# Performance work log

Measured on AMD Instinct MI355X. Metric: run time of the kernel, lower is better.

Reference implementation:

```python
import jax, jax.numpy as jnp
import numpy as np

N_ITER = 5          # n_iterations
EPS_VAR = 1e-6      # added to var (both in update_likelihoods and after M-step)
EPS = 1e-7          # division guard in M-step


def setup_inputs() -> dict:
    key = jax.random.key(0)
    B, N, K, F = 8, 80000, 5, 20
    k1, k2 = jax.random.split(key)
    data = jax.random.normal(k1, (B, N, F), dtype=jnp.float32)
    # initialize_parameters: means are randomly sampled data points
    idx = jax.random.randint(k2, (B, K), 0, N)
    means = jnp.take_along_axis(data, idx[:, :, None], axis=1)          # [B,K,F]
    variance = jnp.ones((B, K, F), dtype=jnp.float32)                    # covariance_init=1.0
    prior = jnp.full((B, K), 1.0 / K, dtype=jnp.float32)
    return {"data": data, "means": means, "variance": variance, "prior": prior}


def _log_likelihoods(data, means, var, pi):
    # data [B,N,F], means/var [B,K,F], pi [B,K] -> [B,K,N]
    inv_cov = 1.0 / (var + EPS_VAR)                                       # [B,K,F]
    diff = data[:, None, :, :] - means[:, :, None, :]                     # [B,K,N,F]
    maha = jnp.einsum('bknf,bkf->bkn', diff * diff, inv_cov)              # bmm in torch
    coeff = -0.5 * jnp.log(2.0 * np.pi * var).sum(axis=-1)                # [B,K]
    return jnp.log(pi)[:, :, None] + coeff[:, :, None] - 0.5 * maha


def _posteriors(log_lik):
    # stable softmax over the cluster dim (dim=1), identical to update_posteriors
    return jax.nn.softmax(log_lik, axis=1)


def _m_step(post, data):
    # post [B,K,N], data [B,N,F]; weights == 1.0 branch of update_parameters
    n = data.shape[1]
    sizes = post.sum(axis=2, keepdims=True)                               # [B,K,1] cluster sizes
    pi = sizes[..., 0] / n                                                # [B,K]
    pi = pi / jnp.maximum(jnp.abs(pi).sum(axis=-1, keepdims=True), 1e-12) # L1 normalize
    means = jnp.einsum('bkn,bnf->bkf', post, data) / (sizes + EPS)        # [B,K,F]
    diff = data[:, None, :, :] - means[:, :, None, :]                     # [B,K,N,F]
    var = jnp.einsum('bkn,bknf->bkf', post, diff * diff) / (sizes + EPS)
    return means, var, pi


def reference(data, means, variance, prior):
    var, pi = variance, prior
    for _ in range(N_ITER):
        ll = _log_likelihoods(data, means, var, pi)
        post = _posteriors(ll)
        means, var, pi = _m_step(post, data)
        var = var + EPS_VAR
    ll = _log_likelihoods(data, means, var, pi)
    post = _posteriors(ll)
    # outputs permuted to [B, N, K] as in forward()
    return (jnp.transpose(ll, (0, 2, 1)), jnp.transpose(post, (0, 2, 1)), means, var, pi)
```

## Files before the change

### kernel.cpp

```cpp
#include <hip/hip_runtime.h>
#include <math.h>

#define BB 8
#define NPTS 80000
#define KK 5
#define FF 20
#define GG 128
#define TILE 64
#define NTILES (NPTS / TILE)
#define PSTRIDE 48

#define WS_CM 0
#define WS_CV 800
#define WS_CP 1600
#define WS_A  1640
#define WS_D  1680
#define WS_E  2480

#define WAIT_BAR() asm volatile("s_waitcnt lgkmcnt(0)\n\ts_barrier" ::: "memory")

__device__ __forceinline__ void make_coefs(const float* __restrict__ means,
                                           const float* __restrict__ var,
                                           const float* __restrict__ pi,
                                           float* __restrict__ A, float* __restrict__ D,
                                           float* __restrict__ E, int t) {
    if (t < BB * KK) {
        float sumlog = 0.f, summ2 = 0.f;
        for (int f = 0; f < FF; ++f) {
            float v = var[t * FF + f];
            float m = means[t * FF + f];
            float ic = 1.f / (v + 1e-6f);
            sumlog += logf(6.283185307179586f * v);
            summ2  += ic * m * m;
            D[t * FF + f] = ic * m;
            E[t * FF + f] = -0.5f * ic;
        }
        A[t] = logf(pi[t]) - 0.5f * sumlog - 0.5f * summ2;
    }
}

__global__ void prepare_kernel(const float* __restrict__ means, const float* __restrict__ var,
                               const float* __restrict__ pi, float* __restrict__ ws) {
    make_coefs(means, var, pi, ws + WS_A, ws + WS_D, ws + WS_E, (int)threadIdx.x);
}

template <bool WRITE_OUT>
__global__ __launch_bounds__(320) void estep_kernel(const float* __restrict__ data,
                                                    const float* __restrict__ ws,
                                                    float* __restrict__ partials,
                                                    float* __restrict__ out_ll,
                                                    float* __restrict__ out_post) {
    __shared__ float lls[2][KK][TILE];

    const int b    = blockIdx.x / GG;
    const int g    = blockIdx.x % GG;
    const int tid  = threadIdx.x;
    const int w    = __builtin_amdgcn_readfirstlane(tid >> 6);
    const int lane = tid & 63;

    const float* A = ws + WS_A;
    const float* D = ws + WS_D;
    const float* E = ws + WS_E;

    const float Ak = A[b * KK + w];
    float dk[FF], ek[FF];
#pragma unroll
    for (int f = 0; f < FF; ++f) {
        dk[f] = D[(b * KK + w) * FF + f];
        ek[f] = E[(b * KK + w) * FF + f];
    }

    float s0 = 0.f, s1[FF], s2[FF];
    if (!WRITE_OUT) {
#pragma unroll
        for (int f = 0; f < FF; ++f) { s1[f] = 0.f; s2[f] = 0.f; }
    }

    const float* dbase = data + (size_t)b * NPTS * FF;
    int pb = 0;

    for (int t = g; t < NTILES; t += GG) {
        const float* xp = dbase + ((size_t)t * TILE + lane) * FF;
        float4 xa = ((const float4*)xp)[0];
        float4 xb = ((const float4*)xp)[1];
        float4 xc = ((const float4*)xp)[2];
        float4 xd = ((const float4*)xp)[3];
        float4 xe = ((const float4*)xp)[4];

        float pf = 0.f;
        const int tn = t + GG;
        if (tn < NTILES) pf = dbase[((size_t)tn * TILE + lane) * FF];

        float x[FF];
        x[0]=xa.x; x[1]=xa.y; x[2]=xa.z; x[3]=xa.w;
        x[4]=xb.x; x[5]=xb.y; x[6]=xb.z; x[7]=xb.w;
        x[8]=xc.x; x[9]=xc.y; x[10]=xc.z; x[11]=xc.w;
        x[12]=xd.x; x[13]=xd.y; x[14]=xd.z; x[15]=xd.w;
        x[16]=xe.x; x[17]=xe.y; x[18]=xe.z; x[19]=xe.w;

        float za = 0.f, zb = 0.f;
#pragma unroll
        for (int f = 0; f < FF; f += 2) {
            za = fmaf(x[f],     fmaf(ek[f],     x[f],     dk[f]),     za);
            zb = fmaf(x[f + 1], fmaf(ek[f + 1], x[f + 1], dk[f + 1]), zb);
        }
        float z = Ak + za + zb;

        lls[pb][w][lane] = z;
        WAIT_BAR();

        float l0 = lls[pb][0][lane], l1 = lls[pb][1][lane], l2 = lls[pb][2][lane],
              l3 = lls[pb][3][lane], l4 = lls[pb][4][lane];
        float mx = fmaxf(fmaxf(fmaxf(l0, l1), fmaxf(l2, l3)), l4);
        float e0 = __expf(l0 - mx), e1 = __expf(l1 - mx), e2 = __expf(l2 - mx),
              e3 = __expf(l3 - mx), e4 = __expf(l4 - mx);
        float inv = 1.f / (e0 + e1 + e2 + e3 + e4);
        float ew  = (w == 0) ? e0 : (w == 1) ? e1 : (w == 2) ? e2 : (w == 3) ? e3 : e4;
        float post = ew * inv;

        if (WRITE_OUT) {
            size_t o = ((size_t)b * NPTS + (size_t)t * TILE + lane) * KK + w;
            out_ll[o]   = z;
            out_post[o] = post;
        } else {
            s0 += post;
#pragma unroll
            for (int f = 0; f < FF; ++f) {
                float px = post * x[f];
                s1[f] += px;
                s2[f] = fmaf(px, x[f], s2[f]);
            }
        }
        asm volatile("" :: "v"(pf));
        pb ^= 1;
    }

    if (!WRITE_OUT) {
#pragma unroll
        for (int off = 32; off > 0; off >>= 1) {
            s0 += __shfl_down(s0, off);
#pragma unroll
            for (int f = 0; f < FF; ++f) {
                s1[f] += __shfl_down(s1[f], off);
                s2[f] += __shfl_down(s2[f], off);
            }
        }
        if (lane == 0) {
            float* row = partials + ((size_t)(b * KK + w) * GG + g) * PSTRIDE;
#pragma unroll
            for (int f = 0; f < FF; ++f) { row[f] = s1[f]; row[FF + f] = s2[f]; }
            row[2 * FF] = s0;
        }
    }
}

__global__ __launch_bounds__(512) void update_kernel(const float* __restrict__ partials,
                                                     float* __restrict__ ws,
                                                     float* __restrict__ om,
                                                     float* __restrict__ ov,
                                                     float* __restrict__ op,
                                                     int write_params) {
    __shared__ float shA[8][PSTRIDE];
    __shared__ float shB[8 * KK];
    const int bk   = blockIdx.x;
    const int b    = bk / KK;
    const int tid  = threadIdx.x;
    const int w8   = tid >> 6;
    const int lane = tid & 63;

    if (lane < PSTRIDE) {
        const float* base = partials + (size_t)bk * GG * PSTRIDE + lane;
        float sv = 0.f;
        for (int gg = w8; gg < GG; gg += 8) sv += base[(size_t)gg * PSTRIDE];
        shA[w8][lane] = sv;
    }
    if (tid < 8 * KK) {
        const int kp = tid >> 3, j = tid & 7;
        const float* cb = partials + (size_t)(b * KK + kp) * GG * PSTRIDE + 2 * FF;
        float s = 0.f;
        for (int gg = j; gg < GG; gg += 8) s += cb[(size_t)gg * PSTRIDE];
        shB[tid] = s;
    }
    __syncthreads();

    if (tid < 64) {
        float svt = 0.f;
        if (lane < PSTRIDE) {
            svt = (shA[0][lane] + shA[1][lane]) + (shA[2][lane] + shA[3][lane])
                + (shA[4][lane] + shA[5][lane]) + (shA[6][lane] + shA[7][lane]);
        }

        float tb = (lane < 8 * KK) ? shB[lane] : 0.f;
#pragma unroll
        for (int off = 32; off > 0; off >>= 1) tb += __shfl_xor(tb, off);

        float s0  = __shfl(svt, 2 * FF);
        float den = s0 + 1e-7f;
        float m   = svt / den;
        float s2f = __shfl(svt, FF + (lane % FF));
        float var = (s2f - 2.f * m * svt + m * m * s0) / den + 1e-6f;

        float* cm = ws + WS_CM; float* cv = ws + WS_CV; float* cp = ws + WS_CP;
        if (lane < FF) {
            cm[bk * FF + lane] = m;
            cv[bk * FF + lane] = var;
            if (write_params) { om[bk * FF + lane] = m; ov[bk * FF + lane] = var; }
        }

        float pr = (s0 / (float)NPTS) / fmaxf(tb / (float)NPTS, 1e-12f);
        if (lane == 0) {
            cp[bk] = pr;
            if (write_params) op[bk] = pr;
        }

        float ic = 1.f / (var + 1e-6f);
        if (lane < FF) {
            (ws + WS_D)[bk * FF + lane] = ic * m;
            (ws + WS_E)[bk * FF + lane] = -0.5f * ic;
        }
        float t1 = (lane < FF) ? logf(6.283185307179586f * var) : 0.f;
        float t2 = (lane < FF) ? ic * m * m : 0.f;
#pragma unroll
        for (int off = 1; off < 64; off <<= 1) {
            t1 += __shfl_xor(t1, off);
            t2 += __shfl_xor(t2, off);
        }
        if (lane == 0)
            (ws + WS_A)[bk] = logf(pr) - 0.5f * t1 - 0.5f * t2;
    }
}

extern "C" void kernel_launch(void* const* d_in, const int* in_sizes, int n_in,
                              void* d_out, int out_size, void* d_ws, size_t ws_size,
                              hipStream_t stream) {
    const float* data     = (const float*)d_in[0];
    const float* in_means = (const float*)d_in[1];
    const float* in_var   = (const float*)d_in[2];
    const float* in_pi    = (const float*)d_in[3];
    float* ws  = (float*)d_ws;
    float* out = (float*)d_out;

    float* out_ll   = out;
    float* out_post = out + (size_t)BB * NPTS * KK;
    float* om       = out + 2 * (size_t)BB * NPTS * KK;
    float* ov       = om + BB * KK * FF;
    float* op       = ov + BB * KK * FF;

    float* partials = out_ll;

    prepare_kernel<<<1, 64, 0, stream>>>(in_means, in_var, in_pi, ws);

    for (int it = 0; it < 5; ++it) {
        estep_kernel<false><<<BB * GG, 320, 0, stream>>>(data, ws, partials,
                                                         nullptr, nullptr);
        update_kernel<<<BB * KK, 512, 0, stream>>>(partials, ws, om, ov, op,
                                                   (it == 4) ? 1 : 0);
    }
    estep_kernel<true><<<BB * GG, 320, 0, stream>>>(data, ws, nullptr,
                                                    out_ll, out_post);
}
```

Before: 327.7 us.

## Fuse M-step reduction into E-step prologue and process two points per lane

Each E-step block now reduces the previous iteration's partial sums itself and computes its own mixture coefficients into shared memory. This drops the separate prepare kernel and four of the five update kernel launches, using ping-pong partial buffers. The tile grows to 128 so each lane handles two points per iteration for more ILP. The cost is that every block redundantly re-reduces the 128 partial rows for its batch, and register pressure rises from holding two point vectors.

```diff
diff --git a/kernel.cpp b/kernel.cpp
--- a/kernel.cpp
+++ b/kernel.cpp
@@ -6,7 +6,7 @@
 #define KK 5
 #define FF 20
 #define GG 128
-#define TILE 64
+#define TILE 128
 #define NTILES (NPTS / TILE)
 #define PSTRIDE 48
 
@@ -19,59 +19,109 @@
 
 #define WAIT_BAR() asm volatile("s_waitcnt lgkmcnt(0)\n\ts_barrier" ::: "memory")
 
-__device__ __forceinline__ void make_coefs(const float* __restrict__ means,
-                                           const float* __restrict__ var,
-                                           const float* __restrict__ pi,
-                                           float* __restrict__ A, float* __restrict__ D,
-                                           float* __restrict__ E, int t) {
-    if (t < BB * KK) {
-        float sumlog = 0.f, summ2 = 0.f;
-        for (int f = 0; f < FF; ++f) {
-            float v = var[t * FF + f];
-            float m = means[t * FF + f];
-            float ic = 1.f / (v + 1e-6f);
-            sumlog += logf(6.283185307179586f * v);
-            summ2  += ic * m * m;
-            D[t * FF + f] = ic * m;
-            E[t * FF + f] = -0.5f * ic;
-        }
-        A[t] = logf(pi[t]) - 0.5f * sumlog - 0.5f * summ2;
-    }
+__device__ __forceinline__ float rfl(float x) {
+    return __uint_as_float(__builtin_amdgcn_readfirstlane(__float_as_uint(x)));
 }
 
-__global__ void prepare_kernel(const float* __restrict__ means, const float* __restrict__ var,
-                               const float* __restrict__ pi, float* __restrict__ ws) {
-    make_coefs(means, var, pi, ws + WS_A, ws + WS_D, ws + WS_E, (int)threadIdx.x);
-}
-
-template <bool WRITE_OUT>
-__global__ __launch_bounds__(320) void estep_kernel(const float* __restrict__ data,
-                                                    const float* __restrict__ ws,
-                                                    float* __restrict__ partials,
-                                                    float* __restrict__ out_ll,
-                                                    float* __restrict__ out_post) {
+template <int MODE>
+__global__ __launch_bounds__(320) void estep_kernel(
+        const float* __restrict__ data,
+        const float* __restrict__ in_means, const float* __restrict__ in_var,
+        const float* __restrict__ in_pi,
+        const float* __restrict__ ws,
+        const float* __restrict__ pin, float* __restrict__ pout,
+        float* __restrict__ out_ll, float* __restrict__ out_post) {
     __shared__ float lls[2][KK][TILE];
+    __shared__ float coefs[KK][2 * FF + 1];
+    __shared__ float s0s[KK];
 
     const int b    = blockIdx.x / GG;
     const int g    = blockIdx.x % GG;
     const int tid  = threadIdx.x;
     const int w    = __builtin_amdgcn_readfirstlane(tid >> 6);
     const int lane = tid & 63;
-
-    const float* A = ws + WS_A;
-    const float* D = ws + WS_D;
-    const float* E = ws + WS_E;
-
-    const float Ak = A[b * KK + w];
+    const int bk   = b * KK + w;
+
     float dk[FF], ek[FF];
-#pragma unroll
-    for (int f = 0; f < FF; ++f) {
-        dk[f] = D[(b * KK + w) * FF + f];
-        ek[f] = E[(b * KK + w) * FF + f];
-    }
-
-    float s0 = 0.f, s1[FF], s2[FF];
-    if (!WRITE_OUT) {
+    float Ak;
+
+    if (MODE == 3) {
+        Ak = (ws + WS_A)[bk];
+#pragma unroll
+        for (int f = 0; f < FF; ++f) {
+            dk[f] = (ws + WS_D)[bk * FF + f];
+            ek[f] = (ws + WS_E)[bk * FF + f];
+        }
+    } else {
+        if (MODE == 0) {
+            float t1 = 0.f, t2 = 0.f;
+            if (lane < FF) {
+                float v = in_var[bk * FF + lane];
+                float m = in_means[bk * FF + lane];
+                float ic = 1.f / (v + 1e-6f);
+                coefs[w][lane]      = ic * m;
+                coefs[w][FF + lane] = -0.5f * ic;
+                t1 = logf(6.283185307179586f * v);
+                t2 = ic * m * m;
+            }
+#pragma unroll
+            for (int off = 1; off < 64; off <<= 1) {
+                t1 += __shfl_xor(t1, off);
+                t2 += __shfl_xor(t2, off);
+            }
+            if (lane == 0)
+                coefs[w][2 * FF] = logf(in_pi[bk]) - 0.5f * t1 - 0.5f * t2;
+            __syncthreads();
+        } else {
+            float sv = 0.f;
+            if (lane < PSTRIDE) {
+                const float* base = pin + (size_t)bk * GG * PSTRIDE + lane;
+                float a0 = 0.f, a1 = 0.f, a2 = 0.f, a3 = 0.f;
+                for (int gg = 0; gg < GG; gg += 4) {
+                    a0 += base[(size_t)(gg    ) * PSTRIDE];
+                    a1 += base[(size_t)(gg + 1) * PSTRIDE];
+                    a2 += base[(size_t)(gg + 2) * PSTRIDE];
+                    a3 += base[(size_t)(gg + 3) * PSTRIDE];
+                }
+                sv = (a0 + a1) + (a2 + a3);
+            }
+            float s0 = __shfl(sv, 2 * FF);
+            if (lane == 0) s0s[w] = s0;
+            __syncthreads();
+            float tot = s0s[0] + s0s[1] + s0s[2] + s0s[3] + s0s[4];
+            float den = s0 + 1e-7f;
+            float m   = sv / den;
+            float s2f = __shfl(sv, FF + (lane % FF));
+            float var = (s2f - 2.f * m * sv + m * m * s0) / den + 1e-6f;
+            float pr  = (s0 / (float)NPTS) / fmaxf(tot / (float)NPTS, 1e-12f);
+            float ic  = 1.f / (var + 1e-6f);
+            float t1 = 0.f, t2 = 0.f;
+            if (lane < FF) {
+                coefs[w][lane]      = ic * m;
+                coefs[w][FF + lane] = -0.5f * ic;
+                t1 = logf(6.283185307179586f * var);
+                t2 = ic * m * m;
+            }
+#pragma unroll
+            for (int off = 1; off < 64; off <<= 1) {
+                t1 += __shfl_xor(t1, off);
+                t2 += __shfl_xor(t2, off);
+            }
+            if (lane == 0)
+                coefs[w][2 * FF] = logf(pr) - 0.5f * t1 - 0.5f * t2;
+            __syncthreads();
+        }
+#pragma unroll
+        for (int f = 0; f < FF; ++f) {
+            dk[f] = rfl(coefs[w][f]);
+            ek[f] = rfl(coefs[w][FF + f]);
+        }
+        Ak = rfl(coefs[w][2 * FF]);
+    }
+
+    constexpr bool ACC = (MODE != 3);
+    float s0a = 0.f, s1[FF], s2[FF];
+    if (ACC) {
 #pragma unroll
         for (int f = 0; f < FF; ++f) { s1[f] = 0.f; s2[f] = 0.f; }
     }
@@ -80,65 +130,92 @@
     int pb = 0;
 
     for (int t = g; t < NTILES; t += GG) {
-        const float* xp = dbase + ((size_t)t * TILE + lane) * FF;
-        float4 xa = ((const float4*)xp)[0];
-        float4 xb = ((const float4*)xp)[1];
-        float4 xc = ((const float4*)xp)[2];
-        float4 xd = ((const float4*)xp)[3];
-        float4 xe = ((const float4*)xp)[4];
-
-        float pf = 0.f;
+        const float* xpA = dbase + ((size_t)t * TILE + lane) * FF;
+        const float* xpB = xpA + 64 * FF;
+        float4 a0 = ((const float4*)xpA)[0];
+        float4 a1 = ((const float4*)xpA)[1];
+        float4 a2 = ((const float4*)xpA)[2];
+        float4 a3 = ((const float4*)xpA)[3];
+        float4 a4 = ((const float4*)xpA)[4];
+        float4 c0 = ((const float4*)xpB)[0];
+        float4 c1 = ((const float4*)xpB)[1];
+        float4 c2 = ((const float4*)xpB)[2];
+        float4 c3 = ((const float4*)xpB)[3];
+        float4 c4 = ((const float4*)xpB)[4];
+
+        float pfA = 0.f, pfB = 0.f;
         const int tn = t + GG;
-        if (tn < NTILES) pf = dbase[((size_t)tn * TILE + lane) * FF];
-
-        float x[FF];
-        x[0]=xa.x; x[1]=xa.y; x[2]=xa.z; x[3]=xa.w;
-        x[4]=xb.x; x[5]=xb.y; x[6]=xb.z; x[7]=xb.w;
-        x[8]=xc.x; x[9]=xc.y; x[10]=xc.z; x[11]=xc.w;
-        x[12]=xd.x; x[13]=xd.y; x[14]=xd.z; x[15]=xd.w;
-        x[16]=xe.x; x[17]=xe.y; x[18]=xe.z; x[19]=xe.w;
-
-        float za = 0.f, zb = 0.f;
-#pragma unroll
-        for (int f = 0; f < FF; f += 2) {
-            za = fmaf(x[f],     fmaf(ek[f],     x[f],     dk[f]),     za);
-            zb = fmaf(x[f + 1], fmaf(ek[f + 1], x[f + 1], dk[f + 1]), zb);
-        }
-        float z = Ak + za + zb;
-
-        lls[pb][w][lane] = z;
+        if (tn < NTILES) {
+            pfA = dbase[((size_t)tn * TILE + lane) * FF];
+            pfB = dbase[((size_t)tn * TILE + 64 + lane) * FF];
+        }
+
+        float xA[FF], xB[FF];
+        xA[0]=a0.x; xA[1]=a0.y; xA[2]=a0.z; xA[3]=a0.w;
+        xA[4]=a1.x; xA[5]=a1.y; xA[6]=a1.z; xA[7]=a1.w;
+        xA[8]=a2.x; xA[9]=a2.y; xA[10]=a2.z; xA[11]=a2.w;
+        xA[12]=a3.x; xA[13]=a3.y; xA[14]=a3.z; xA[15]=a3.w;
+        xA[16]=a4.x; xA[17]=a4.y; xA[18]=a4.z; xA[19]=a4.w;
+        xB[0]=c0.x; xB[1]=c0.y; xB[2]=c0.z; xB[3]=c0.w;
+        xB[4]=c1.x; xB[5]=c1.y; xB[6]=c1.z; xB[7]=c1.w;
+        xB[8]=c2.x; xB[9]=c2.y; xB[10]=c2.z; xB[11]=c2.w;
+        xB[12]=c3.x; xB[13]=c3.y; xB[14]=c3.z; xB[15]=c3.w;
+        xB[16]=c4.x; xB[17]=c4.y; xB[18]=c4.z; xB[19]=c4.w;
+
+        float zA = Ak, zB = Ak;
+#pragma unroll
+        for (int f = 0; f < FF; ++f) {
+            zA = fmaf(xA[f], fmaf(ek[f], xA[f], dk[f]), zA);
+            zB = fmaf(xB[f], fmaf(ek[f], xB[f], dk[f]), zB);
+        }
+        lls[pb][w][lane]      = zA;
+        lls[pb][w][lane + 64] = zB;
         WAIT_BAR();
 
         float l0 = lls[pb][0][lane], l1 = lls[pb][1][lane], l2 = lls[pb][2][lane],
               l3 = lls[pb][3][lane], l4 = lls[pb][4][lane];
-        float mx = fmaxf(fmaxf(fmaxf(l0, l1), fmaxf(l2, l3)), l4);
-        float e0 = __expf(l0 - mx), e1 = __expf(l1 - mx), e2 = __expf(l2 - mx),
-              e3 = __expf(l3 - mx), e4 = __expf(l4 - mx);
-        float inv = 1.f / (e0 + e1 + e2 + e3 + e4);
-        float ew  = (w == 0) ? e0 : (w == 1) ? e1 : (w == 2) ? e2 : (w == 3) ? e3 : e4;
-        float post = ew * inv;
-
-        if (WRITE_OUT) {
-            size_t o = ((size_t)b * NPTS + (size_t)t * TILE + lane) * KK + w;
-            out_ll[o]   = z;
-            out_post[o] = post;
+        float mxA = fmaxf(fmaxf(fmaxf(l0, l1), fmaxf(l2, l3)), l4);
+        float e0 = __expf(l0 - mxA), e1 = __expf(l1 - mxA), e2 = __expf(l2 - mxA),
+              e3 = __expf(l3 - mxA), e4 = __expf(l4 - mxA);
+        float invA = 1.f / (e0 + e1 + e2 + e3 + e4);
+        float ewA  = (w == 0) ? e0 : (w == 1) ? e1 : (w == 2) ? e2 : (w == 3) ? e3 : e4;
+        float postA = ewA * invA;
+
+        float m0 = lls[pb][0][lane+64], m1 = lls[pb][1][lane+64], m2 = lls[pb][2][lane+64],
+              m3 = lls[pb][3][lane+64], m4 = lls[pb][4][lane+64];
+        float mxB = fmaxf(fmaxf(fmaxf(m0, m1), fmaxf(m2, m3)), m4);
+        float f0 = __expf(m0 - mxB), f1 = __expf(m1 - mxB), f2 = __expf(m2 - mxB),
+              f3 = __expf(m3 - mxB), f4 = __expf(m4 - mxB);
+        float invB = 1.f / (f0 + f1 + f2 + f3 + f4);
+        float ewB  = (w == 0) ? f0 : (w == 1) ? f1 : (w == 2) ? f2 : (w == 3) ? f3 : f4;
+        float postB = ewB * invB;
+
+        if (!ACC) {
+            size_t oA = ((size_t)b * NPTS + (size_t)t * TILE + lane) * KK + w;
+            out_ll[oA]   = zA;
+            out_post[oA] = postA;
+            size_t oB = oA + (size_t)64 * KK;
+            out_ll[oB]   = zB;
+            out_post[oB] = postB;
         } else {
-            s0 += post;
+            s0a += postA + postB;
 #pragma unroll
             for (int f = 0; f < FF; ++f) {
-                float px = post * x[f];
-                s1[f] += px;
-                s2[f] = fmaf(px, x[f], s2[f]);
-            }
-        }
-        asm volatile("" :: "v"(pf));
+                float qA = postA * xA[f];
+                float qB = postB * xB[f];
+                s1[f] += qA + qB;
+                s2[f] = fmaf(qA, xA[f], s2[f]);
+                s2[f] = fmaf(qB, xB[f], s2[f]);
+            }
+        }
+        asm volatile("" :: "v"(pfA), "v"(pfB));
         pb ^= 1;
     }
 
-    if (!WRITE_OUT) {
+    if (ACC) {
 #pragma unroll
         for (int off = 32; off > 0; off >>= 1) {
-            s0 += __shfl_down(s0, off);
+            s0a += __shfl_down(s0a, off);
 #pragma unroll
             for (int f = 0; f < FF; ++f) {
                 s1[f] += __shfl_down(s1[f], off);
@@ -146,10 +223,10 @@
             }
         }
         if (lane == 0) {
-            float* row = partials + ((size_t)(b * KK + w) * GG + g) * PSTRIDE;
+            float* row = pout + ((size_t)bk * GG + g) * PSTRIDE;
 #pragma unroll
             for (int f = 0; f < FF; ++f) { row[f] = s1[f]; row[FF + f] = s2[f]; }
-            row[2 * FF] = s0;
+            row[2 * FF] = s0a;
         }
     }
 }
@@ -158,8 +235,7 @@
                                                      float* __restrict__ ws,
                                                      float* __restrict__ om,
                                                      float* __restrict__ ov,
-                                                     float* __restrict__ op,
-                                                     int write_params) {
+                                                     float* __restrict__ op) {
     __shared__ float shA[8][PSTRIDE];
     __shared__ float shB[8 * KK];
     const int bk   = blockIdx.x;
@@ -200,18 +276,13 @@
         float s2f = __shfl(svt, FF + (lane % FF));
         float var = (s2f - 2.f * m * svt + m * m * s0) / den + 1e-6f;
 
-        float* cm = ws + WS_CM; float* cv = ws + WS_CV; float* cp = ws + WS_CP;
         if (lane < FF) {
-            cm[bk * FF + lane] = m;
-            cv[bk * FF + lane] = var;
-            if (write_params) { om[bk * FF + lane] = m; ov[bk * FF + lane] = var; }
+            om[bk * FF + lane] = m;
+            ov[bk * FF + lane] = var;
         }
 
         float pr = (s0 / (float)NPTS) / fmaxf(tb / (float)NPTS, 1e-12f);
-        if (lane == 0) {
-            cp[bk] = pr;
-            if (write_params) op[bk] = pr;
-        }
+        if (lane == 0) op[bk] = pr;
 
         float ic = 1.f / (var + 1e-6f);
         if (lane < FF) {
@@ -246,16 +317,20 @@
     float* ov       = om + BB * KK * FF;
     float* op       = ov + BB * KK * FF;
 
-    float* partials = out_ll;
-
-    prepare_kernel<<<1, 64, 0, stream>>>(in_means, in_var, in_pi, ws);
-
-    for (int it = 0; it < 5; ++it) {
-        estep_kernel<false><<<BB * GG, 320, 0, stream>>>(data, ws, partials,
-                                                         nullptr, nullptr);
-        update_kernel<<<BB * KK, 512, 0, stream>>>(partials, ws, om, ov, op,
-                                                   (it == 4) ? 1 : 0);
-    }
-    estep_kernel<true><<<BB * GG, 320, 0, stream>>>(data, ws, nullptr,
-                                                    out_ll, out_post);
+    float* P0 = out_ll;
+    float* P1 = out_ll + 262144;
+
+    estep_kernel<0><<<BB * GG, 320, 0, stream>>>(data, in_means, in_var, in_pi,
+                                                 ws, nullptr, P0, nullptr, nullptr);
+    estep_kernel<1><<<BB * GG, 320, 0, stream>>>(data, nullptr, nullptr, nullptr,
+                                                 ws, P0, P1, nullptr, nullptr);
+    estep_kernel<1><<<BB * GG, 320, 0, stream>>>(data, nullptr, nullptr, nullptr,
+                                                 ws, P1, P0, nullptr, nullptr);
+    estep_kernel<1><<<BB * GG, 320, 0, stream>>>(data, nullptr, nullptr, nullptr,
+                                                 ws, P0, P1, nullptr, nullptr);
+    estep_kernel<1><<<BB * GG, 320, 0, stream>>>(data, nullptr, nullptr, nullptr,
+                                                 ws, P1, P0, nullptr, nullptr);
+    update_kernel<<<BB * KK, 512, 0, stream>>>(P0, ws, om, ov, op);
+    estep_kernel<3><<<BB * GG, 320, 0, stream>>>(data, nullptr, nullptr, nullptr,
+                                                 ws, nullptr, nullptr, out_ll, out_post);
 }
```

Result: slower. 352.4 us (+7.5%).

## Map 12 points x 5 clusters per wavefront and softmax via shuffles

Applied to the files above, without the earlier changes.

The E-step kernel now assigns each wavefront 12 points across all 5 clusters (60 active lanes), so the softmax over clusters uses cross-lane shuffles instead of LDS plus a block barrier. The first iteration computes its coefficients inline from the input parameters, which removes the separate prepare kernel. The update kernel also stops writing the unused current-parameter copies. In exchange, 4 of every 64 lanes sit idle, each thread loads whole points, and there are four times as many partial rows to reduce.

```diff
diff --git a/kernel.cpp b/kernel.cpp
--- a/kernel.cpp
+++ b/kernel.cpp
@@ -5,82 +5,77 @@
 #define NPTS 80000
 #define KK 5
 #define FF 20
-#define GG 128
-#define TILE 64
-#define NTILES (NPTS / TILE)
+#define GB 128
+#define WPB (GB * 4)
+#define PPT 12
+#define NT12 ((NPTS + PPT - 1) / PPT)
 #define PSTRIDE 48
 
-#define WS_CM 0
-#define WS_CV 800
-#define WS_CP 1600
-#define WS_A  1640
-#define WS_D  1680
-#define WS_E  2480
-
-#define WAIT_BAR() asm volatile("s_waitcnt lgkmcnt(0)\n\ts_barrier" ::: "memory")
-
-__device__ __forceinline__ void make_coefs(const float* __restrict__ means,
-                                           const float* __restrict__ var,
-                                           const float* __restrict__ pi,
-                                           float* __restrict__ A, float* __restrict__ D,
-                                           float* __restrict__ E, int t) {
-    if (t < BB * KK) {
+#define WS_A  0
+#define WS_D  40
+#define WS_E  840
+
+template <int MODE>
+__global__ __launch_bounds__(256) void estep_kernel(
+        const float* __restrict__ data,
+        const float* __restrict__ in_means, const float* __restrict__ in_var,
+        const float* __restrict__ in_pi,
+        const float* __restrict__ ws,
+        float* __restrict__ pout,
+        float* __restrict__ out_ll, float* __restrict__ out_post) {
+    const int b    = blockIdx.x / GB;
+    const int blk  = blockIdx.x % GB;
+    const int tid  = threadIdx.x;
+    const int lane = tid & 63;
+    const int wv   = blk * 4 + (tid >> 6);
+    const int g    = lane / PPT;
+    const int j    = lane % PPT;
+    const bool act = (g < KK);
+    const int gc   = act ? g : KK - 1;
+    const int bk   = b * KK + gc;
+
+    float dk[FF], ek[FF], Ak;
+    if (MODE == 0) {
         float sumlog = 0.f, summ2 = 0.f;
+#pragma unroll
         for (int f = 0; f < FF; ++f) {
-            float v = var[t * FF + f];
-            float m = means[t * FF + f];
+            float v = in_var[bk * FF + f];
+            float m = in_means[bk * FF + f];
             float ic = 1.f / (v + 1e-6f);
+            dk[f] = ic * m;
+            ek[f] = -0.5f * ic;
             sumlog += logf(6.283185307179586f * v);
             summ2  += ic * m * m;
-            D[t * FF + f] = ic * m;
-            E[t * FF + f] = -0.5f * ic;
-        }
-        A[t] = logf(pi[t]) - 0.5f * sumlog - 0.5f * summ2;
-    }
-}
-
-__global__ void prepare_kernel(const float* __restrict__ means, const float* __restrict__ var,
-                               const float* __restrict__ pi, float* __restrict__ ws) {
-    make_coefs(means, var, pi, ws + WS_A, ws + WS_D, ws + WS_E, (int)threadIdx.x);
-}
-
-template <bool WRITE_OUT>
-__global__ __launch_bounds__(320) void estep_kernel(const float* __restrict__ data,
-                                                    const float* __restrict__ ws,
-                                                    float* __restrict__ partials,
-                                                    float* __restrict__ out_ll,
-                                                    float* __restrict__ out_post) {
-    __shared__ float lls[2][KK][TILE];
-
-    const int b    = blockIdx.x / GG;
-    const int g    = blockIdx.x % GG;
-    const int tid  = threadIdx.x;
-    const int w    = __builtin_amdgcn_readfirstlane(tid >> 6);
-    const int lane = tid & 63;
-
-    const float* A = ws + WS_A;
-    const float* D = ws + WS_D;
-    const float* E = ws + WS_E;
-
-    const float Ak = A[b * KK + w];
-    float dk[FF], ek[FF];
-#pragma unroll
-    for (int f = 0; f < FF; ++f) {
-        dk[f] = D[(b * KK + w) * FF + f];
-        ek[f] = E[(b * KK + w) * FF + f];
-    }
-
-    float s0 = 0.f, s1[FF], s2[FF];
-    if (!WRITE_OUT) {
+        }
+        Ak = logf(in_pi[bk]) - 0.5f * sumlog - 0.5f * summ2;
+    } else {
+        Ak = (ws + WS_A)[bk];
+#pragma unroll
+        for (int f = 0; f < FF; ++f) {
+            dk[f] = (ws + WS_D)[bk * FF + f];
+            ek[f] = (ws + WS_E)[bk * FF + f];
+        }
+    }
+
+    const int src1 = j + PPT * ((g + 1) % KK);
+    const int src2 = j + PPT * ((g + 2) % KK);
+    const int src3 = j + PPT * ((g + 3) % KK);
+    const int src4 = j + PPT * ((g + 4) % KK);
+
+    constexpr bool ACC = (MODE != 3);
+    float s0a = 0.f, s1[FF], s2[FF];
+    if (ACC) {
 #pragma unroll
         for (int f = 0; f < FF; ++f) { s1[f] = 0.f; s2[f] = 0.f; }
     }
 
     const float* dbase = data + (size_t)b * NPTS * FF;
-    int pb = 0;
-
-    for (int t = g; t < NTILES; t += GG) {
-        const float* xp = dbase + ((size_t)t * TILE + lane) * FF;
+    float pf_hold = 0.f;
+
+    for (int t = wv; t < NT12; t += WPB) {
+        const int p  = t * PPT + j;
+        const int pc = (p < NPTS) ? p : (NPTS - 1);
+        const float* xp = dbase + (size_t)pc * FF;
         float4 xa = ((const float4*)xp)[0];
         float4 xb = ((const float4*)xp)[1];
         float4 xc = ((const float4*)xp)[2];
@@ -88,8 +83,12 @@
         float4 xe = ((const float4*)xp)[4];
 
         float pf = 0.f;
-        const int tn = t + GG;
-        if (tn < NTILES) pf = dbase[((size_t)tn * TILE + lane) * FF];
+        const int tn = t + WPB;
+        if (tn < NT12) {
+            int pn = tn * PPT + j;
+            if (pn >= NPTS) pn = NPTS - 1;
+            pf = dbase[(size_t)pn * FF];
+        }
 
         float x[FF];
         x[0]=xa.x; x[1]=xa.y; x[2]=xa.z; x[3]=xa.w;
@@ -104,26 +103,31 @@
             za = fmaf(x[f],     fmaf(ek[f],     x[f],     dk[f]),     za);
             zb = fmaf(x[f + 1], fmaf(ek[f + 1], x[f + 1], dk[f + 1]), zb);
         }
-        float z = Ak + za + zb;
-
-        lls[pb][w][lane] = z;
-        WAIT_BAR();
-
-        float l0 = lls[pb][0][lane], l1 = lls[pb][1][lane], l2 = lls[pb][2][lane],
-              l3 = lls[pb][3][lane], l4 = lls[pb][4][lane];
-        float mx = fmaxf(fmaxf(fmaxf(l0, l1), fmaxf(l2, l3)), l4);
-        float e0 = __expf(l0 - mx), e1 = __expf(l1 - mx), e2 = __expf(l2 - mx),
-              e3 = __expf(l3 - mx), e4 = __expf(l4 - mx);
-        float inv = 1.f / (e0 + e1 + e2 + e3 + e4);
-        float ew  = (w == 0) ? e0 : (w == 1) ? e1 : (w == 2) ? e2 : (w == 3) ? e3 : e4;
-        float post = ew * inv;
-
-        if (WRITE_OUT) {
-            size_t o = ((size_t)b * NPTS + (size_t)t * TILE + lane) * KK + w;
-            out_ll[o]   = z;
-            out_post[o] = post;
+        const float z = Ak + za + zb;
+
+        float mx = z;
+        mx = fmaxf(mx, __shfl(z, src1));
+        mx = fmaxf(mx, __shfl(z, src2));
+        mx = fmaxf(mx, __shfl(z, src3));
+        mx = fmaxf(mx, __shfl(z, src4));
+        const float e = __expf(z - mx);
+        float sum = e;
+        sum += __shfl(e, src1);
+        sum += __shfl(e, src2);
+        sum += __shfl(e, src3);
+        sum += __shfl(e, src4);
+        float post = e / sum;
+
+        const bool valid = act && (p < NPTS);
+        if (!ACC) {
+            if (valid) {
+                size_t o = ((size_t)b * NPTS + p) * KK + g;
+                out_ll[o]   = z;
+                out_post[o] = post;
+            }
         } else {
-            s0 += post;
+            post = valid ? post : 0.f;
+            s0a += post;
 #pragma unroll
             for (int f = 0; f < FF; ++f) {
                 float px = post * x[f];
@@ -131,25 +135,23 @@
                 s2[f] = fmaf(px, x[f], s2[f]);
             }
         }
-        asm volatile("" :: "v"(pf));
-        pb ^= 1;
-    }
-
-    if (!WRITE_OUT) {
-#pragma unroll
-        for (int off = 32; off > 0; off >>= 1) {
-            s0 += __shfl_down(s0, off);
-#pragma unroll
-            for (int f = 0; f < FF; ++f) {
-                s1[f] += __shfl_down(s1[f], off);
-                s2[f] += __shfl_down(s2[f], off);
-            }
-        }
-        if (lane == 0) {
-            float* row = partials + ((size_t)(b * KK + w) * GG + g) * PSTRIDE;
+        asm volatile("" :: "v"(pf_hold));
+        pf_hold = pf;
+    }
+    asm volatile("" :: "v"(pf_hold));
+
+    if (ACC) {
+#define RED12(v) { float _t1 = __shfl_down(v, 4), _t2 = __shfl_down(v, 8); \
+                   v += _t1 + _t2; v += __shfl_down(v, 2); v += __shfl_down(v, 1); }
+        RED12(s0a);
+#pragma unroll
+        for (int f = 0; f < FF; ++f) { RED12(s1[f]); RED12(s2[f]); }
+#undef RED12
+        if (act && j == 0) {
+            float* row = pout + ((size_t)bk * WPB + wv) * PSTRIDE;
 #pragma unroll
             for (int f = 0; f < FF; ++f) { row[f] = s1[f]; row[FF + f] = s2[f]; }
-            row[2 * FF] = s0;
+            row[2 * FF] = s0a;
         }
     }
 }
@@ -169,16 +171,19 @@
     const int lane = tid & 63;
 
     if (lane < PSTRIDE) {
-        const float* base = partials + (size_t)bk * GG * PSTRIDE + lane;
-        float sv = 0.f;
-        for (int gg = w8; gg < GG; gg += 8) sv += base[(size_t)gg * PSTRIDE];
-        shA[w8][lane] = sv;
+        const float* base = partials + (size_t)bk * WPB * PSTRIDE + lane;
+        float a0 = 0.f, a1 = 0.f;
+        for (int gg = w8; gg < WPB; gg += 16) {
+            a0 += base[(size_t)gg * PSTRIDE];
+            a1 += base[(size_t)(gg + 8) * PSTRIDE];
+        }
+        shA[w8][lane] = a0 + a1;
     }
     if (tid < 8 * KK) {
-        const int kp = tid >> 3, j = tid & 7;
-        const float* cb = partials + (size_t)(b * KK + kp) * GG * PSTRIDE + 2 * FF;
+        const int kp = tid >> 3, jx = tid & 7;
+        const float* cb = partials + (size_t)(b * KK + kp) * WPB * PSTRIDE + 2 * FF;
         float s = 0.f;
-        for (int gg = j; gg < GG; gg += 8) s += cb[(size_t)gg * PSTRIDE];
+        for (int gg = jx; gg < WPB; gg += 8) s += cb[(size_t)gg * PSTRIDE];
         shB[tid] = s;
     }
     __syncthreads();
@@ -200,18 +205,13 @@
         float s2f = __shfl(svt, FF + (lane % FF));
         float var = (s2f - 2.f * m * svt + m * m * s0) / den + 1e-6f;
 
-        float* cm = ws + WS_CM; float* cv = ws + WS_CV; float* cp = ws + WS_CP;
-        if (lane < FF) {
-            cm[bk * FF + lane] = m;
-            cv[bk * FF + lane] = var;
-            if (write_params) { om[bk * FF + lane] = m; ov[bk * FF + lane] = var; }
+        if (write_params && lane < FF) {
+            om[bk * FF + lane] = m;
+            ov[bk * FF + lane] = var;
         }
 
         float pr = (s0 / (float)NPTS) / fmaxf(tb / (float)NPTS, 1e-12f);
-        if (lane == 0) {
-            cp[bk] = pr;
-            if (write_params) op[bk] = pr;
-        }
+        if (write_params && lane == 0) op[bk] = pr;
 
         float ic = 1.f / (var + 1e-6f);
         if (lane < FF) {
@@ -246,16 +246,16 @@
     float* ov       = om + BB * KK * FF;
     float* op       = ov + BB * KK * FF;
 
-    float* partials = out_ll;
-
-    prepare_kernel<<<1, 64, 0, stream>>>(in_means, in_var, in_pi, ws);
-
-    for (int it = 0; it < 5; ++it) {
-        estep_kernel<false><<<BB * GG, 320, 0, stream>>>(data, ws, partials,
-                                                         nullptr, nullptr);
-        update_kernel<<<BB * KK, 512, 0, stream>>>(partials, ws, om, ov, op,
-                                                   (it == 4) ? 1 : 0);
-    }
-    estep_kernel<true><<<BB * GG, 320, 0, stream>>>(data, ws, nullptr,
-                                                    out_ll, out_post);
+    float* P = out_ll;
+
+    estep_kernel<0><<<BB * GB, 256, 0, stream>>>(data, in_means, in_var, in_pi,
+                                                 ws, P, nullptr, nullptr);
+    for (int it = 1; it < 5; ++it) {
+        update_kernel<<<BB * KK, 512, 0, stream>>>(P, ws, om, ov, op, 0);
+        estep_kernel<1><<<BB * GB, 256, 0, stream>>>(data, nullptr, nullptr, nullptr,
+                                                     ws, P, nullptr, nullptr);
+    }
+    update_kernel<<<BB * KK, 512, 0, stream>>>(P, ws, om, ov, op, 1);
+    estep_kernel<3><<<BB * GB, 256, 0, stream>>>(data, nullptr, nullptr, nullptr,
+                                                 ws, nullptr, out_ll, out_post);
 }
```

Result: slower. 367.3 us (+12.1%).

## Stage data tiles into LDS with async global_load_lds ring buffer

Applied to the files above, without the earlier changes.

Before this change, each of the five cluster waves in a block loaded the same 64x20 data tile from global memory on its own. Now each tile is loaded once per block straight into shared memory with global_load_lds. A 4-slot ring buffer prefetches two tiles ahead, and the waits and barrier use vmcnt so loads overlap compute. This is meant to cut the redundant global and L2 traffic and hide load latency. The cost is more LDS per block, which may lower occupancy, plus added LDS reads in both the likelihood pass and the accumulation pass. Unused workspace copies of the means, variances and priors are also dropped from the update kernel.

```diff
diff --git a/kernel.cpp b/kernel.cpp
--- a/kernel.cpp
+++ b/kernel.cpp
@@ -10,20 +10,18 @@
 #define NTILES (NPTS / TILE)
 #define PSTRIDE 48
 
-#define WS_CM 0
-#define WS_CV 800
-#define WS_CP 1600
-#define WS_A  1640
-#define WS_D  1680
-#define WS_E  2480
-
-#define WAIT_BAR() asm volatile("s_waitcnt lgkmcnt(0)\n\ts_barrier" ::: "memory")
-
-__device__ __forceinline__ void make_coefs(const float* __restrict__ means,
-                                           const float* __restrict__ var,
-                                           const float* __restrict__ pi,
-                                           float* __restrict__ A, float* __restrict__ D,
-                                           float* __restrict__ E, int t) {
+#define WS_A  0
+#define WS_D  40
+#define WS_E  840
+
+#define STAGE(ldsp, gp)                                                        \
+    __builtin_amdgcn_global_load_lds(                                          \
+        (const __attribute__((address_space(1))) void*)(const void*)(gp),      \
+        (__attribute__((address_space(3))) void*)(void*)(ldsp), 16, 0, 0)
+
+__global__ void prepare_kernel(const float* __restrict__ means, const float* __restrict__ var,
+                               const float* __restrict__ pi, float* __restrict__ ws) {
+    int t = (int)threadIdx.x;
     if (t < BB * KK) {
         float sumlog = 0.f, summ2 = 0.f;
         for (int f = 0; f < FF; ++f) {
@@ -32,16 +30,11 @@
             float ic = 1.f / (v + 1e-6f);
             sumlog += logf(6.283185307179586f * v);
             summ2  += ic * m * m;
-            D[t * FF + f] = ic * m;
-            E[t * FF + f] = -0.5f * ic;
-        }
-        A[t] = logf(pi[t]) - 0.5f * sumlog - 0.5f * summ2;
-    }
-}
-
-__global__ void prepare_kernel(const float* __restrict__ means, const float* __restrict__ var,
-                               const float* __restrict__ pi, float* __restrict__ ws) {
-    make_coefs(means, var, pi, ws + WS_A, ws + WS_D, ws + WS_E, (int)threadIdx.x);
+            (ws + WS_D)[t * FF + f] = ic * m;
+            (ws + WS_E)[t * FF + f] = -0.5f * ic;
+        }
+        (ws + WS_A)[t] = logf(pi[t]) - 0.5f * sumlog - 0.5f * summ2;
+    }
 }
 
 template <bool WRITE_OUT>
@@ -50,6 +43,7 @@
                                                     float* __restrict__ partials,
                                                     float* __restrict__ out_ll,
                                                     float* __restrict__ out_post) {
+    __shared__ float xs[4][TILE * FF];
     __shared__ float lls[2][KK][TILE];
 
     const int b    = blockIdx.x / GG;
@@ -58,16 +52,12 @@
     const int w    = __builtin_amdgcn_readfirstlane(tid >> 6);
     const int lane = tid & 63;
 
-    const float* A = ws + WS_A;
-    const float* D = ws + WS_D;
-    const float* E = ws + WS_E;
-
-    const float Ak = A[b * KK + w];
+    const float Ak = (ws + WS_A)[b * KK + w];
     float dk[FF], ek[FF];
 #pragma unroll
     for (int f = 0; f < FF; ++f) {
-        dk[f] = D[(b * KK + w) * FF + f];
-        ek[f] = E[(b * KK + w) * FF + f];
+        dk[f] = (ws + WS_D)[(b * KK + w) * FF + f];
+        ek[f] = (ws + WS_E)[(b * KK + w) * FF + f];
     }
 
     float s0 = 0.f, s1[FF], s2[FF];
@@ -77,37 +67,41 @@
     }
 
     const float* dbase = data + (size_t)b * NPTS * FF;
-    int pb = 0;
-
+    const int toff = tid * 4;
+
+    STAGE(&xs[0][toff], dbase + (size_t)g * TILE * FF + toff);
+    STAGE(&xs[1][toff], dbase + (size_t)(g + GG) * TILE * FF + toff);
+    asm volatile("s_waitcnt vmcnt(0)" ::: "memory");
+    __syncthreads();
+
+    int cur = 0, pb = 0;
     for (int t = g; t < NTILES; t += GG) {
-        const float* xp = dbase + ((size_t)t * TILE + lane) * FF;
-        float4 xa = ((const float4*)xp)[0];
-        float4 xb = ((const float4*)xp)[1];
-        float4 xc = ((const float4*)xp)[2];
-        float4 xd = ((const float4*)xp)[3];
-        float4 xe = ((const float4*)xp)[4];
-
-        float pf = 0.f;
-        const int tn = t + GG;
-        if (tn < NTILES) pf = dbase[((size_t)tn * TILE + lane) * FF];
-
-        float x[FF];
-        x[0]=xa.x; x[1]=xa.y; x[2]=xa.z; x[3]=xa.w;
-        x[4]=xb.x; x[5]=xb.y; x[6]=xb.z; x[7]=xb.w;
-        x[8]=xc.x; x[9]=xc.y; x[10]=xc.z; x[11]=xc.w;
-        x[12]=xd.x; x[13]=xd.y; x[14]=xd.z; x[15]=xd.w;
-        x[16]=xe.x; x[17]=xe.y; x[18]=xe.z; x[19]=xe.w;
-
+        const int t2 = t + 2 * GG;
+        if (t2 < NTILES) {
+            const int nx2 = (cur + 2) & 3;
+            STAGE(&xs[nx2][toff], dbase + (size_t)t2 * TILE * FF + toff);
+        }
+
+        const float4* xr = (const float4*)&xs[cur][lane * FF];
+        float4 v0 = xr[0], v1 = xr[1], v2 = xr[2], v3 = xr[3], v4 = xr[4];
+        float xz[FF];
+        xz[0]=v0.x; xz[1]=v0.y; xz[2]=v0.z; xz[3]=v0.w;
+        xz[4]=v1.x; xz[5]=v1.y; xz[6]=v1.z; xz[7]=v1.w;
+        xz[8]=v2.x; xz[9]=v2.y; xz[10]=v2.z; xz[11]=v2.w;
+        xz[12]=v3.x; xz[13]=v3.y; xz[14]=v3.z; xz[15]=v3.w;
+        xz[16]=v4.x; xz[17]=v4.y; xz[18]=v4.z; xz[19]=v4.w;
         float za = 0.f, zb = 0.f;
 #pragma unroll
         for (int f = 0; f < FF; f += 2) {
-            za = fmaf(x[f],     fmaf(ek[f],     x[f],     dk[f]),     za);
-            zb = fmaf(x[f + 1], fmaf(ek[f + 1], x[f + 1], dk[f + 1]), zb);
-        }
-        float z = Ak + za + zb;
-
-        lls[pb][w][lane] = z;
-        WAIT_BAR();
+            za = fmaf(xz[f],     fmaf(ek[f],     xz[f],     dk[f]),     za);
+            zb = fmaf(xz[f + 1], fmaf(ek[f + 1], xz[f + 1], dk[f + 1]), zb);
+        }
+        lls[pb][w][lane] = Ak + za + zb;
+
+        if (t2 < NTILES)
+            asm volatile("s_waitcnt vmcnt(1) lgkmcnt(0)\n\ts_barrier" ::: "memory");
+        else
+            asm volatile("s_waitcnt vmcnt(0) lgkmcnt(0)\n\ts_barrier" ::: "memory");
 
         float l0 = lls[pb][0][lane], l1 = lls[pb][1][lane], l2 = lls[pb][2][lane],
               l3 = lls[pb][3][lane], l4 = lls[pb][4][lane];
@@ -117,6 +111,7 @@
         float inv = 1.f / (e0 + e1 + e2 + e3 + e4);
         float ew  = (w == 0) ? e0 : (w == 1) ? e1 : (w == 2) ? e2 : (w == 3) ? e3 : e4;
         float post = ew * inv;
+        float z = (w == 0) ? l0 : (w == 1) ? l1 : (w == 2) ? l2 : (w == 3) ? l3 : l4;
 
         if (WRITE_OUT) {
             size_t o = ((size_t)b * NPTS + (size_t)t * TILE + lane) * KK + w;
@@ -124,14 +119,19 @@
             out_post[o] = post;
         } else {
             s0 += post;
-#pragma unroll
-            for (int f = 0; f < FF; ++f) {
-                float px = post * x[f];
-                s1[f] += px;
-                s2[f] = fmaf(px, x[f], s2[f]);
+            const float4* xr2 = (const float4*)&xs[cur][lane * FF];
+#pragma unroll
+            for (int j = 0; j < 5; ++j) {
+                float4 u = xr2[j];
+                float p0 = post * u.x, p1 = post * u.y,
+                      p2 = post * u.z, p3 = post * u.w;
+                s1[4*j]   += p0;  s2[4*j]   = fmaf(p0, u.x, s2[4*j]);
+                s1[4*j+1] += p1;  s2[4*j+1] = fmaf(p1, u.y, s2[4*j+1]);
+                s1[4*j+2] += p2;  s2[4*j+2] = fmaf(p2, u.z, s2[4*j+2]);
+                s1[4*j+3] += p3;  s2[4*j+3] = fmaf(p3, u.w, s2[4*j+3]);
             }
         }
-        asm volatile("" :: "v"(pf));
+        cur = (cur + 1) & 3;
         pb ^= 1;
     }
 
@@ -200,18 +200,13 @@
         float s2f = __shfl(svt, FF + (lane % FF));
         float var = (s2f - 2.f * m * svt + m * m * s0) / den + 1e-6f;
 
-        float* cm = ws + WS_CM; float* cv = ws + WS_CV; float* cp = ws + WS_CP;
-        if (lane < FF) {
-            cm[bk * FF + lane] = m;
-            cv[bk * FF + lane] = var;
-            if (write_params) { om[bk * FF + lane] = m; ov[bk * FF + lane] = var; }
+        if (write_params && lane < FF) {
+            om[bk * FF + lane] = m;
+            ov[bk * FF + lane] = var;
         }
 
         float pr = (s0 / (float)NPTS) / fmaxf(tb / (float)NPTS, 1e-12f);
-        if (lane == 0) {
-            cp[bk] = pr;
-            if (write_params) op[bk] = pr;
-        }
+        if (write_params && lane == 0) op[bk] = pr;
 
         float ic = 1.f / (var + 1e-6f);
         if (lane < FF) {
@@ -246,14 +241,14 @@
     float* ov       = om + BB * KK * FF;
     float* op       = ov + BB * KK * FF;
 
-    float* partials = out_ll;
+    float* P = out_ll;
 
     prepare_kernel<<<1, 64, 0, stream>>>(in_means, in_var, in_pi, ws);
 
     for (int it = 0; it < 5; ++it) {
-        estep_kernel<false><<<BB * GG, 320, 0, stream>>>(data, ws, partials,
+        estep_kernel<false><<<BB * GG, 320, 0, stream>>>(data, ws, P,
                                                          nullptr, nullptr);
-        update_kernel<<<BB * KK, 512, 0, stream>>>(partials, ws, om, ov, op,
+        update_kernel<<<BB * KK, 512, 0, stream>>>(P, ws, om, ov, op,
                                                    (it == 4) ? 1 : 0);
     }
     estep_kernel<true><<<BB * GG, 320, 0, stream>>>(data, ws, nullptr,
```

Measured after the change: 319.3 us. -2.6%, faster.
